# Kernel optimization log

Measured on AMD Instinct MI355X. Metric: run time of the kernel, lower is better.

The kernel has to match this reference:

```python
import jax, jax.numpy as jnp
import numpy as np
from jax import lax

GRID_W, GRID_H = 4, 4
N_NODES = GRID_W * GRID_H  # 16
N_NEIGH = 8
N_CLS = 10
BN_EPS = 1e-5


def _neighbors(i, w, h, mode=8):
    # exact port of Brain.neighbors (ordering matters for the concat)
    size = w * h
    out = []
    if i - w >= 0:
        out.append(i - w)
    if i % w != 0:
        out.append(i - 1)
    if (i + 1) % w != 0:
        out.append(i + 1)
    if i + w < size:
        out.append(i + w)
    if mode == 8:
        if i - w - 1 >= 0 and i % w != 0:
            out.append(i - w - 1)
        if i - w + 1 >= 0 and (i + 1) % w != 0:
            out.append(i - w + 1)
        if i + w - 1 < size and i % w != 0:
            out.append(i + w - 1)
        if i + w + 1 < size and (i + 1) % w != 0:
            out.append(i + w + 1)
    return out


def _neighbor_table():
    idx = np.full((N_NODES, N_NEIGH), 0, dtype=np.int32)
    mask = np.zeros((N_NODES, N_NEIGH), dtype=np.float32)
    for i in range(N_NODES):
        n = _neighbors(i, GRID_W, GRID_H, 8)
        idx[i, :len(n)] = np.array(n, dtype=np.int32)
        mask[i, :len(n)] = 1.0
    return jnp.asarray(idx), jnp.asarray(mask)


def _conv(x, w, b):
    y = lax.conv_general_dilated(x, w, (1, 1), 'SAME',
                                 dimension_numbers=('NCHW', 'OIHW', 'NCHW'))
    return y + b[None, :, None, None]


def _bn_train(x, g, b):
    # BatchNorm2d in training mode (module default): batch statistics
    mean = jnp.mean(x, axis=(0, 2, 3), keepdims=True)
    var = jnp.var(x, axis=(0, 2, 3), keepdims=True)
    xn = (x - mean) * lax.rsqrt(var + BN_EPS)
    return xn * g[None, :, None, None] + b[None, :, None, None]


def _maxpool(x):
    # MaxPool2d(kernel=3, stride=2, padding=1)
    return lax.reduce_window(x, -jnp.inf, lax.max,
                             (1, 1, 3, 3), (1, 1, 2, 2),
                             ((0, 0), (0, 0), (1, 1), (1, 1)))


def setup_inputs() -> dict:
    key = jax.random.key(0)
    ks = jax.random.split(key, 24)
    B = 128
    f32 = jnp.float32

    def rn(k, shape, scale):
        return jax.random.normal(k, shape, dtype=f32) * scale

    inp = {
        'x': rn(ks[0], (B, 3, 64, 64), 1.0),
        'cw1': rn(ks[1], (64, 3, 3, 3), 0.1), 'cb1': jnp.zeros((64,), f32),
        'bn1_g': jnp.ones((64,), f32), 'bn1_b': jnp.zeros((64,), f32),
        'cw2': rn(ks[2], (128, 64, 3, 3), 0.05), 'cb2': jnp.zeros((128,), f32),
        'bn2_g': jnp.ones((128,), f32), 'bn2_b': jnp.zeros((128,), f32),
        'cw3': rn(ks[3], (256, 128, 3, 3), 0.03), 'cb3': jnp.zeros((256,), f32),
        'cw4': rn(ks[4], (256, 256, 3, 3), 0.02), 'cb4': jnp.zeros((256,), f32),
        'cw5': rn(ks[5], (512, 256, 3, 3), 0.02), 'cb5': jnp.zeros((512,), f32),
        'cw6': rn(ks[6], (512, 512, 3, 3), 0.015), 'cb6': jnp.zeros((512,), f32),
        'cw7': rn(ks[7], (512, 512, 3, 3), 0.015), 'cb7': jnp.zeros((512,), f32),
        'W1': rn(ks[8], (N_NODES, 592, 600), 0.04), 'b1': jnp.zeros((N_NODES, 600), f32),
        'W2': rn(ks[9], (N_NODES, 600, N_CLS), 0.04), 'b2': jnp.zeros((N_NODES, N_CLS), f32),
    }
    return inp


def _backbone(x, cw1, cb1, bn1_g, bn1_b, cw2, cb2, bn2_g, bn2_b,
              cw3, cb3, cw4, cb4, cw5, cb5, cw6, cb6, cw7, cb7):
    h = _maxpool(jax.nn.relu(_bn_train(_conv(x, cw1, cb1), bn1_g, bn1_b)))
    h = _maxpool(jax.nn.relu(_bn_train(_conv(h, cw2, cb2), bn2_g, bn2_b)))
    h = jax.nn.relu(_conv(h, cw3, cb3))
    h = _maxpool(jax.nn.relu(_conv(h, cw4, cb4)))
    h = jax.nn.relu(_conv(h, cw5, cb5))
    h = _maxpool(jax.nn.relu(_conv(h, cw6, cb6)))
    h = jax.nn.relu(_conv(h, cw7, cb7))
    return h  # [B, 512, 4, 4]


def _colons(X, W1, b1, W2, b2):
    # X: [16, B, 592] -> softmax probs [16, B, 10]; per-node MLP
    h = jnp.tanh(jnp.einsum('nbi,nio->nbo', X, W1) + b1[:, None, :])
    logits = jnp.einsum('nbh,nho->nbo', h, W2) + b2[:, None, :]
    return jax.nn.softmax(logits, axis=-1)


def reference(x, cw1, cb1, bn1_g, bn1_b, cw2, cb2, bn2_g, bn2_b,
              cw3, cb3, cw4, cb4, cw5, cb5, cw6, cb6, cw7, cb7,
              W1, b1, W2, b2):
    B = x.shape[0]
    conv = _backbone(x, cw1, cb1, bn1_g, bn1_b, cw2, cb2, bn2_g, bn2_b,
                     cw3, cb3, cw4, cb4, cw5, cb5, cw6, cb6, cw7, cb7)
    conv = conv.reshape(B, 512, N_NODES)           # torch.flatten(conv, 2)
    feats = jnp.transpose(conv, (2, 0, 1))         # [16, B, 512]

    # first pass: neighbor slots are all-zero p1..p8
    zeros80 = jnp.zeros((N_NODES, B, N_NEIGH * N_CLS), dtype=x.dtype)
    preds1 = _colons(jnp.concatenate([zeros80, feats], axis=-1), W1, b1, W2, b2)

    # second pass: gather neighbor predictions (zero-padded to 8 slots)
    idx, mask = _neighbor_table()                  # [16,8] int, [16,8] float
    gathered = preds1[idx]                         # [16, 8, B, 10]
    gathered = gathered * mask[:, :, None, None]
    neigh = jnp.transpose(gathered, (0, 2, 1, 3)).reshape(N_NODES, B, N_NEIGH * N_CLS)
    preds2 = _colons(jnp.concatenate([neigh, feats], axis=-1), W1, b1, W2, b2)  # [16, B, 10]

    sum_preds = jnp.mean(preds2, axis=0)           # [B, 10]
    squared_sum_preds = sum_preds * sum_preds
    return squared_sum_preds, preds2
```

## Files before the change

kernel.cpp:

```cpp
#include <hip/hip_runtime.h>
#include <math.h>


#define BN_EPS 1e-5f

typedef _Float16 f16x8 __attribute__((ext_vector_type(8)));
typedef _Float16 f16x4 __attribute__((ext_vector_type(4)));
typedef float    f32x4v __attribute__((ext_vector_type(4)));

constexpr int ilog2c(int x) { return x <= 1 ? 0 : 1 + ilog2c(x >> 1); }

__global__ __launch_bounds__(256)
void wsplit_kernel(const float* __restrict__ w, _Float16* __restrict__ o, int COCI)
{
    const int t = blockIdx.x * 256 + threadIdx.x;
    if (t >= COCI) return;
#pragma unroll
    for (int ph = 0; ph < 9; ++ph)
        o[ph * COCI + t] = (_Float16)w[t * 9 + ph];
}

__global__ void wsplit1_kernel(const float* __restrict__ w, _Float16* __restrict__ o)
{
    const int co = threadIdx.x;
#pragma unroll
    for (int k = 0; k < 32; ++k)
        o[co * 32 + k] = (k < 27) ? (_Float16)w[co * 27 + k] : (_Float16)0.f;
}

__global__ __launch_bounds__(256)
void conv1_mfma_kernel(const float* __restrict__ in, const _Float16* __restrict__ w32,
                       _Float16* __restrict__ out, int B)
{
    __shared__ __align__(16) _Float16 As[64 * 32];
    __shared__ __align__(16) _Float16 Bs[128 * 32];

    const int tid  = threadIdx.x;
    const int pix0 = blockIdx.x * 128;
    const int bn   = tid & 127;
    const int bh   = tid >> 7;
    const int gp   = pix0 + bn;
    const int pb   = gp >> 12;
    const int sp   = gp & 4095;
    const int py   = sp >> 6;
    const int px   = sp & 63;
    const float* inb = in + (size_t)pb * 3 * 4096;

    _Float16 vals[16];
    if (bh == 0) {
#pragma unroll
        for (int u = 0; u < 16; ++u) {
            const int k = u;
            const int ci = k / 9, r = k - ci * 9, ky = r / 3, kx = r - ky * 3;
            const int iy = py + ky - 1, ix = px + kx - 1;
            float v = 0.f;
            if ((unsigned)iy < 64u && (unsigned)ix < 64u)
                v = inb[ci * 4096 + iy * 64 + ix];
            vals[u] = (_Float16)v;
        }
    } else {
#pragma unroll
        for (int u = 0; u < 16; ++u) {
            const int k = 16 + u;
            float v = 0.f;
            if (k < 27) {
                const int ci = k / 9, r = k - ci * 9, ky = r / 3, kx = r - ky * 3;
                const int iy = py + ky - 1, ix = px + kx - 1;
                if ((unsigned)iy < 64u && (unsigned)ix < 64u)
                    v = inb[ci * 4096 + iy * 64 + ix];
            }
            vals[u] = (_Float16)v;
        }
    }
    f16x8 b0, b1;
#pragma unroll
    for (int j = 0; j < 8; ++j) { b0[j] = vals[j]; b1[j] = vals[8 + j]; }
    *(f16x8*)&Bs[bn * 32 + (((2 * bh    ) ^ (bn & 3)) << 3)] = b0;
    *(f16x8*)&Bs[bn * 32 + (((2 * bh + 1) ^ (bn & 3)) << 3)] = b1;

    if (tid < 128) {
        const int arow = tid >> 1, ah = tid & 1;
        const f16x8 a0 = *(const f16x8*)(w32 + arow * 32 + ah * 16);
        const f16x8 a1 = *(const f16x8*)(w32 + arow * 32 + ah * 16 + 8);
        *(f16x8*)&As[arow * 32 + (((2 * ah    ) ^ (arow & 3)) << 3)] = a0;
        *(f16x8*)&As[arow * 32 + (((2 * ah + 1) ^ (arow & 3)) << 3)] = a1;
    }
    __syncthreads();

    const int lane = tid & 63, wv = tid >> 6;
    const int q = lane >> 4, lm = lane & 15;
    const int swz = (q ^ (lm & 3)) << 3;

    f16x8 af[4], bf[2];
#pragma unroll
    for (int ti = 0; ti < 4; ++ti)
        af[ti] = *(const f16x8*)&As[(ti * 16 + lm) * 32 + swz];
#pragma unroll
    for (int tj = 0; tj < 2; ++tj)
        bf[tj] = *(const f16x8*)&Bs[(wv * 32 + tj * 16 + lm) * 32 + swz];

    f32x4v acc[4][2];
#pragma unroll
    for (int ti = 0; ti < 4; ++ti)
#pragma unroll
        for (int tj = 0; tj < 2; ++tj)
            acc[ti][tj] = __builtin_amdgcn_mfma_f32_16x16x32_f16(
                af[ti], bf[tj], (f32x4v)0.f, 0, 0, 0);

#pragma unroll
    for (int tj = 0; tj < 2; ++tj) {
        const int gpix = pix0 + wv * 32 + tj * 16 + lm;
#pragma unroll
        for (int ti = 0; ti < 4; ++ti) {
            const int cob = ti * 16 + q * 4;
            f16x4 h4;
#pragma unroll
            for (int r = 0; r < 4; ++r) h4[r] = (_Float16)acc[ti][tj][r];
            *(f16x4*)&out[(size_t)gpix * 64 + cob] = h4;
        }
    }
}

template <int CI, int CO, int H, int W, int KSPLIT, int EPI>
__global__ __launch_bounds__(256)
void conv_nhwc_kernel(const _Float16* __restrict__ in, const _Float16* __restrict__ w9,
                      const float* __restrict__ bias, _Float16* __restrict__ out,
                      float* __restrict__ part, int B)
{
    constexpr int HW   = H * W;
    constexpr int lgHW = ilog2c(HW);
    constexpr int lgW  = ilog2c(W);

    __shared__ __align__(16) _Float16 As[128 * 32];
    __shared__ __align__(16) _Float16 Bs[128 * 32];

    const int tid  = threadIdx.x;
    const int pix0 = blockIdx.x * 128;
    const int co0  = blockIdx.y * 128;

    const int bn = tid & 127;
    const int bh = tid >> 7;
    const int gp = pix0 + bn;
    const int pb = gp >> lgHW;
    const int sp = gp & (HW - 1);
    const int py = sp >> lgW;
    const int px = sp & (W - 1);

    const int arow = tid >> 1;
    const int ah   = tid & 1;

    const int lane = tid & 63, wv = tid >> 6;
    const int wm = (wv & 1) * 64;
    const int wn = (wv >> 1) * 64;
    const int q = lane >> 4, lm = lane & 15;
    const int swz = (q ^ (lm & 3)) << 3;

    const int bw0 = ((2 * bh    ) ^ (bn & 3)) << 3;
    const int bw1 = ((2 * bh + 1) ^ (bn & 3)) << 3;
    const int aw0 = ((2 * ah    ) ^ (arow & 3)) << 3;
    const int aw1 = ((2 * ah + 1) ^ (arow & 3)) << 3;

    f32x4v acc[4][4];
#pragma unroll
    for (int i = 0; i < 4; ++i)
#pragma unroll
        for (int j = 0; j < 4; ++j) acc[i][j] = (f32x4v)0.f;

    constexpr int CS_TOT = CI / 32;
    constexpr int CS_PER = CS_TOT / KSPLIT;
    const int cs0 = (KSPLIT > 1) ? blockIdx.z * CS_PER : 0;

    for (int ph = 0; ph < 9; ++ph) {
        const int dy = ph / 3 - 1;
        const int dx = ph - (ph / 3) * 3 - 1;
        const int y2 = py + dy;
        const int x2 = px + dx;
        const bool valid = ((unsigned)y2 < (unsigned)H) && ((unsigned)x2 < (unsigned)W);
        const _Float16 msk = valid ? (_Float16)1.f : (_Float16)0.f;
        const int sp2 = valid ? ((y2 << lgW) | x2) : 0;
        const _Float16* bsrc = in + ((size_t)((pb << lgHW) | sp2)) * CI + bh * 16;
        const _Float16* asrc = w9 + ((size_t)(ph * CO) + co0 + arow) * CI + ah * 16;

        for (int cs = cs0; cs < cs0 + CS_PER; ++cs) {
            f16x8 bv0 = *(const f16x8*)(bsrc + cs * 32);
            f16x8 bv1 = *(const f16x8*)(bsrc + cs * 32 + 8);
            const f16x8 av0 = *(const f16x8*)(asrc + cs * 32);
            const f16x8 av1 = *(const f16x8*)(asrc + cs * 32 + 8);

            __syncthreads();
            bv0 *= msk;
            bv1 *= msk;
            *(f16x8*)&Bs[bn * 32 + bw0]   = bv0;
            *(f16x8*)&Bs[bn * 32 + bw1]   = bv1;
            *(f16x8*)&As[arow * 32 + aw0] = av0;
            *(f16x8*)&As[arow * 32 + aw1] = av1;
            __syncthreads();

            f16x8 af[4], bf[4];
#pragma unroll
            for (int ti = 0; ti < 4; ++ti)
                af[ti] = *(const f16x8*)&As[(wm + ti * 16 + lm) * 32 + swz];
#pragma unroll
            for (int tj = 0; tj < 4; ++tj)
                bf[tj] = *(const f16x8*)&Bs[(wn + tj * 16 + lm) * 32 + swz];
#pragma unroll
            for (int ti = 0; ti < 4; ++ti)
#pragma unroll
                for (int tj = 0; tj < 4; ++tj)
                    acc[ti][tj] = __builtin_amdgcn_mfma_f32_16x16x32_f16(
                        af[ti], bf[tj], acc[ti][tj], 0, 0, 0);
        }
    }

    if (EPI == 2) {
        float* pout = part + (size_t)blockIdx.z * ((size_t)B * HW * CO);
#pragma unroll
        for (int tj = 0; tj < 4; ++tj) {
            const int gpix = pix0 + wn + tj * 16 + lm;
#pragma unroll
            for (int ti = 0; ti < 4; ++ti) {
                const int cob = co0 + wm + ti * 16 + q * 4;
                *(float4*)&pout[(size_t)gpix * CO + cob] =
                    make_float4(acc[ti][tj][0], acc[ti][tj][1],
                                acc[ti][tj][2], acc[ti][tj][3]);
            }
        }
    } else {
#pragma unroll
        for (int tj = 0; tj < 4; ++tj) {
            const int gpix = pix0 + wn + tj * 16 + lm;
#pragma unroll
            for (int ti = 0; ti < 4; ++ti) {
                const int cob = co0 + wm + ti * 16 + q * 4;
                f16x4 h4;
                if (EPI == 1) {
                    const float4 bb = *(const float4*)&bias[cob];
                    h4[0] = (_Float16)fmaxf(acc[ti][tj][0] + bb.x, 0.f);
                    h4[1] = (_Float16)fmaxf(acc[ti][tj][1] + bb.y, 0.f);
                    h4[2] = (_Float16)fmaxf(acc[ti][tj][2] + bb.z, 0.f);
                    h4[3] = (_Float16)fmaxf(acc[ti][tj][3] + bb.w, 0.f);
                } else {
#pragma unroll
                    for (int r = 0; r < 4; ++r) h4[r] = (_Float16)acc[ti][tj][r];
                }
                *(f16x4*)&out[(size_t)gpix * CO + cob] = h4;
            }
        }
    }
}

template <int C>
__global__ __launch_bounds__(256)
void bn_stats_nhwc_kernel(const _Float16* __restrict__ in, float* __restrict__ sums,
                          int Ptot)
{
    constexpr int C8 = C / 8;
    constexpr int PS = 256 / C8;
    const int chunk = Ptot / gridDim.x;
    const int c8   = threadIdx.x & (C8 - 1);
    const int poff = threadIdx.x >> ilog2c(C8);
    float s[8], s2[8];
#pragma unroll
    for (int j = 0; j < 8; ++j) { s[j] = 0.f; s2[j] = 0.f; }
    const int p0 = blockIdx.x * chunk;
    for (int p = p0 + poff; p < p0 + chunk; p += PS) {
        const f16x8 v = *(const f16x8*)(in + (size_t)p * C + c8 * 8);
#pragma unroll
        for (int j = 0; j < 8; ++j) {
            const float f = (float)v[j];
            s[j] += f; s2[j] += f * f;
        }
    }
    __shared__ float ls[2 * C];
    for (int i = threadIdx.x; i < 2 * C; i += 256) ls[i] = 0.f;
    __syncthreads();
#pragma unroll
    for (int j = 0; j < 8; ++j) {
        atomicAdd(&ls[c8 * 8 + j], s[j]);
        atomicAdd(&ls[C + c8 * 8 + j], s2[j]);
    }
    __syncthreads();
    for (int i = threadIdx.x; i < 2 * C; i += 256) atomicAdd(&sums[i], ls[i]);
}

template <int C>
__global__ void bn_finalize_kernel(const float* __restrict__ sums,
                                   const float* __restrict__ g,
                                   const float* __restrict__ beta,
                                   float* __restrict__ ss, int Ntot)
{
    const int c = blockIdx.x * 64 + threadIdx.x;
    if (c >= C) return;
    const float inv   = 1.f / (float)Ntot;
    const float mean  = sums[c] * inv;
    const float var   = sums[C + c] * inv - mean * mean;
    const float scale = g[c] * rsqrtf(var + BN_EPS);
    ss[c]     = scale;
    ss[C + c] = beta[c] - mean * scale;
}

template <int C, int Hin, int Win, bool DO_BN>
__global__ __launch_bounds__(256)
void pool_nhwc_kernel(const _Float16* __restrict__ in, const float* __restrict__ ss,
                      _Float16* __restrict__ out, int B)
{
    constexpr int Ho = Hin / 2, Wo = Win / 2, C8 = C / 8;
    constexpr int lgC8 = ilog2c(C8), lgWo = ilog2c(Wo), lgHo = ilog2c(Ho);
    const int t = blockIdx.x * 256 + threadIdx.x;
    const int total = B * Ho * Wo * C8;
    if (t >= total) return;
    const int c8 = t & (C8 - 1);
    const int r1 = t >> lgC8;
    const int ox = r1 & (Wo - 1);
    const int r2 = r1 >> lgWo;
    const int oy = r2 & (Ho - 1);
    const int b  = r2 >> lgHo;

    float sc[8], sh[8];
    if (DO_BN) {
#pragma unroll
        for (int j = 0; j < 8; ++j) {
            sc[j] = ss[c8 * 8 + j];
            sh[j] = ss[C + c8 * 8 + j];
        }
    }
    float m[8];
#pragma unroll
    for (int j = 0; j < 8; ++j) m[j] = -1e30f;

    const int y0 = max(0, 2 * oy - 1), y1 = min(Hin - 1, 2 * oy + 1);
    const int x0 = max(0, 2 * ox - 1), x1 = min(Win - 1, 2 * ox + 1);
    const _Float16* ib = in + ((size_t)b * Hin * Win) * C + c8 * 8;
    for (int iy = y0; iy <= y1; ++iy)
        for (int ix = x0; ix <= x1; ++ix) {
            const f16x8 v = *(const f16x8*)(ib + (size_t)(iy * Win + ix) * C);
#pragma unroll
            for (int j = 0; j < 8; ++j) {
                float f = (float)v[j];
                if (DO_BN) f = f * sc[j] + sh[j];
                m[j] = fmaxf(m[j], f);
            }
        }
    f16x8 o;
#pragma unroll
    for (int j = 0; j < 8; ++j) {
        float f = m[j];
        if (DO_BN) f = fmaxf(f, 0.f);
        o[j] = (_Float16)f;
    }
    *(f16x8*)&out[((size_t)((b << (lgHo + lgWo)) | (oy << lgWo) | ox)) * C + c8 * 8] = o;
}

template <int CO, int Z>
__global__ __launch_bounds__(256)
void sum_bias_relu_nhwc_kernel(const float* __restrict__ part, const float* __restrict__ bias,
                               _Float16* __restrict__ out, int Npix)
{
    const int t = blockIdx.x * 256 + threadIdx.x;
    const int N8 = Npix * CO / 8;
    if (t >= N8) return;
    const size_t i8 = (size_t)t * 8;
    const int c = (int)(i8 & (CO - 1));
    const size_t S = (size_t)Npix * CO;
    float4 x0 = *(const float4*)(part + i8);
    float4 x1 = *(const float4*)(part + i8 + 4);
#pragma unroll
    for (int z = 1; z < Z; ++z) {
        const float4 p0 = *(const float4*)(part + z * S + i8);
        const float4 p1 = *(const float4*)(part + z * S + i8 + 4);
        x0.x += p0.x; x0.y += p0.y; x0.z += p0.z; x0.w += p0.w;
        x1.x += p1.x; x1.y += p1.y; x1.z += p1.z; x1.w += p1.w;
    }
    const float4 b0 = *(const float4*)(bias + c);
    const float4 b1 = *(const float4*)(bias + c + 4);
    f16x8 o;
    o[0] = (_Float16)fmaxf(x0.x + b0.x, 0.f);
    o[1] = (_Float16)fmaxf(x0.y + b0.y, 0.f);
    o[2] = (_Float16)fmaxf(x0.z + b0.z, 0.f);
    o[3] = (_Float16)fmaxf(x0.w + b0.w, 0.f);
    o[4] = (_Float16)fmaxf(x1.x + b1.x, 0.f);
    o[5] = (_Float16)fmaxf(x1.y + b1.y, 0.f);
    o[6] = (_Float16)fmaxf(x1.z + b1.z, 0.f);
    o[7] = (_Float16)fmaxf(x1.w + b1.w, 0.f);
    *(f16x8*)&out[i8] = o;
}

template <int Z>
__global__ __launch_bounds__(256)
void build_x_kernel(const float* __restrict__ part, const float* __restrict__ bias,
                    float* __restrict__ X, int B)
{
    const int t = blockIdx.x * 256 + threadIdx.x;
    if (t >= B * 16 * 128) return;
    const int pix = t >> 7;
    const int c   = (t & 127) * 4;
    const size_t S = (size_t)B * 16 * 512;
    float4 a = *(const float4*)(part + (size_t)pix * 512 + c);
#pragma unroll
    for (int z = 1; z < Z; ++z) {
        const float4 p = *(const float4*)(part + z * S + (size_t)pix * 512 + c);
        a.x += p.x; a.y += p.y; a.z += p.z; a.w += p.w;
    }
    const float4 bb = *(const float4*)(bias + c);
    a.x = fmaxf(a.x + bb.x, 0.f);
    a.y = fmaxf(a.y + bb.y, 0.f);
    a.z = fmaxf(a.z + bb.z, 0.f);
    a.w = fmaxf(a.w + bb.w, 0.f);
    const int b_ = pix >> 4, sp = pix & 15;
    *(float4*)&X[((size_t)(sp * B + b_)) * 592 + 80 + c] = a;
}

template <int K, int XOFF, int WOFF, bool WRITE_PRE, bool ADD_PRE>
__global__ __launch_bounds__(256)
void colon_fc1_kernel(const float* __restrict__ X, const float* __restrict__ W1,
                      const float* __restrict__ b1, float* __restrict__ pre,
                      float* __restrict__ h, int B)
{
    constexpr int N = 600, BK = 16;
    const int n  = blockIdx.z;
    const int m0 = blockIdx.y * 64;
    const int o0 = blockIdx.x * 64;

    __shared__ __align__(16) float As[BK][68];
    __shared__ __align__(16) float Bs[BK][68];

    const int tid = threadIdx.x;
    const int tx = tid & 15, ty = tid >> 4;
    const int a_m = tid >> 2, a_k4 = (tid & 3) * 4;
    const int b_o = tid & 63, b_kr = tid >> 6;

    const float* Xn  = X  + (size_t)n * B * 592;
    const float* W1n = W1 + (size_t)n * 592 * N;

    float acc[4][4];
#pragma unroll
    for (int i = 0; i < 4; ++i)
#pragma unroll
        for (int j = 0; j < 4; ++j) acc[i][j] = 0.f;

    for (int kb = 0; kb < K; kb += BK) {
        const float4 av = *reinterpret_cast<const float4*>(
            &Xn[(size_t)(m0 + a_m) * 592 + XOFF + kb + a_k4]);
        As[a_k4 + 0][a_m] = av.x;
        As[a_k4 + 1][a_m] = av.y;
        As[a_k4 + 2][a_m] = av.z;
        As[a_k4 + 3][a_m] = av.w;
#pragma unroll
        for (int i = 0; i < 4; ++i) {
            const int kl = b_kr + i * 4;
            const int o  = o0 + b_o;
            Bs[kl][b_o] = (o < N) ? W1n[(size_t)(WOFF + kb + kl) * N + o] : 0.f;
        }
        __syncthreads();
#pragma unroll
        for (int kk = 0; kk < BK; ++kk) {
            const float4 a4 = *reinterpret_cast<const float4*>(&As[kk][ty * 4]);
            const float4 b4 = *reinterpret_cast<const float4*>(&Bs[kk][tx * 4]);
            const float a0[4] = {a4.x, a4.y, a4.z, a4.w};
            const float b0[4] = {b4.x, b4.y, b4.z, b4.w};
#pragma unroll
            for (int i = 0; i < 4; ++i)
#pragma unroll
                for (int j = 0; j < 4; ++j)
                    acc[i][j] += a0[i] * b0[j];
        }
        __syncthreads();
    }

#pragma unroll
    for (int i = 0; i < 4; ++i) {
        const int m = m0 + ty * 4 + i;
#pragma unroll
        for (int j = 0; j < 4; ++j) {
            const int o = o0 + tx * 4 + j;
            if (o < N) {
                const size_t oi = ((size_t)(n * B + m)) * N + o;
                float v = acc[i][j] + (ADD_PRE ? pre[oi] : b1[n * N + o]);
                if (WRITE_PRE) pre[oi] = v;
                h[oi] = tanhf(v);
            }
        }
    }
}

__global__ __launch_bounds__(128)
void colon_fc2_kernel(const float* __restrict__ h, const float* __restrict__ W2,
                      const float* __restrict__ b2, float* __restrict__ preds, int B)
{
    const int n = blockIdx.x;
    __shared__ float W2s[6000];
    __shared__ float b2s[10];
    for (int i = threadIdx.x; i < 6000; i += 128) W2s[i] = W2[n * 6000 + i];
    if (threadIdx.x < 10) b2s[threadIdx.x] = b2[n * 10 + threadIdx.x];
    __syncthreads();

    for (int b = threadIdx.x; b < B; b += 128) {
        float l[10];
#pragma unroll
        for (int c = 0; c < 10; ++c) l[c] = b2s[c];
        const float* hp = h + ((size_t)(n * B + b)) * 600;
        for (int k = 0; k < 600; k += 4) {
            const float4 hv = *reinterpret_cast<const float4*>(&hp[k]);
            const float hh[4] = {hv.x, hv.y, hv.z, hv.w};
#pragma unroll
            for (int u = 0; u < 4; ++u)
#pragma unroll
                for (int c = 0; c < 10; ++c)
                    l[c] += hh[u] * W2s[(k + u) * 10 + c];
        }
        float mx = l[0];
#pragma unroll
        for (int c = 1; c < 10; ++c) mx = fmaxf(mx, l[c]);
        float s = 0.f;
#pragma unroll
        for (int c = 0; c < 10; ++c) { l[c] = expf(l[c] - mx); s += l[c]; }
        const float inv = 1.f / s;
        float* pp = preds + ((size_t)(n * B + b)) * 10;
#pragma unroll
        for (int c = 0; c < 10; ++c) pp[c] = l[c] * inv;
    }
}

__global__ __launch_bounds__(256)
void fill_neigh_kernel(const float* __restrict__ preds1, float* __restrict__ X, int B)
{
    const int t = blockIdx.x * 256 + threadIdx.x;
    if (t >= 16 * B * 80) return;
    const int c = t % 10;
    const int j = (t / 10) & 7;
    const int b = (t / 80) % B;
    const int n = t / (80 * B);

    int lst[8];
    int cnt = 0;
    const int w = 4, sz = 16, i = n;
    if (i - w >= 0)                                lst[cnt++] = i - w;
    if (i % w != 0)                                lst[cnt++] = i - 1;
    if ((i + 1) % w != 0)                          lst[cnt++] = i + 1;
    if (i + w < sz)                                lst[cnt++] = i + w;
    if (i - w - 1 >= 0 && i % w != 0)              lst[cnt++] = i - w - 1;
    if (i - w + 1 >= 0 && (i + 1) % w != 0)        lst[cnt++] = i - w + 1;
    if (i + w - 1 < sz && i % w != 0)              lst[cnt++] = i + w - 1;
    if (i + w + 1 < sz && (i + 1) % w != 0)        lst[cnt++] = i + w + 1;

    float v = 0.f;
    if (j < cnt) v = preds1[((size_t)(lst[j] * B + b)) * 10 + c];
    X[((size_t)(n * B + b)) * 592 + j * 10 + c] = v;
}

__global__ __launch_bounds__(256)
void final_out_kernel(const float* __restrict__ preds2, float* __restrict__ out0, int B)
{
    const int t = blockIdx.x * 256 + threadIdx.x;
    if (t >= B * 10) return;
    const int b = t / 10, c = t % 10;
    float s = 0.f;
#pragma unroll
    for (int n = 0; n < 16; ++n)
        s += preds2[((size_t)(n * B + b)) * 10 + c];
    const float m = s * (1.f / 16.f);
    out0[t] = m * m;
}

extern "C" void kernel_launch(void* const* d_in, const int* in_sizes, int n_in,
                              void* d_out, int out_size, void* d_ws, size_t ws_size,
                              hipStream_t stream)
{
    const float* x    = (const float*)d_in[0];
    const float* cw1  = (const float*)d_in[1];
    const float* bn1g = (const float*)d_in[3];
    const float* bn1b = (const float*)d_in[4];
    const float* cw2  = (const float*)d_in[5];
    const float* bn2g = (const float*)d_in[7];
    const float* bn2b = (const float*)d_in[8];
    const float* cw3  = (const float*)d_in[9];
    const float* cb3  = (const float*)d_in[10];
    const float* cw4  = (const float*)d_in[11];
    const float* cb4  = (const float*)d_in[12];
    const float* cw5  = (const float*)d_in[13];
    const float* cb5  = (const float*)d_in[14];
    const float* cw6  = (const float*)d_in[15];
    const float* cb6  = (const float*)d_in[16];
    const float* cw7  = (const float*)d_in[17];
    const float* cb7  = (const float*)d_in[18];
    const float* W1   = (const float*)d_in[19];
    const float* b1   = (const float*)d_in[20];
    const float* W2   = (const float*)d_in[21];
    const float* b2   = (const float*)d_in[22];

    const int B = in_sizes[0] / (3 * 64 * 64);

    float* ws = (float*)d_ws;
    float*     P    = ws;
    _Float16*  A    = (_Float16*)(ws + 16777216);
    _Float16*  Bb   = (_Float16*)(ws + 33554432);
    _Float16*  wreg = (_Float16*)(ws + 41943040);
    float*     Xb   = ws + 45371392;
    float*     hb   = ws + 46583808;
    float*     preb = ws + 47812608;
    float*     small= ws + 49041408;
    float* sums1  = small;
    float* sums2  = small + 256;
    float* ss1    = small + 1024;
    float* ss2    = small + 1536;
    float* preds1 = small + 2048;

    _Float16* w1f  = wreg;
    _Float16* w9c2 = wreg + 2048;
    _Float16* w9c3 = w9c2 + 73728;
    _Float16* w9c4 = w9c3 + 294912;
    _Float16* w9c5 = w9c4 + 589824;
    _Float16* w9c6 = w9c5 + 1179648;
    _Float16* w9c7 = w9c6 + 2359296;

    float* out0   = (float*)d_out;
    float* preds2 = (float*)d_out + (size_t)B * 10;

    hipMemsetAsync(small, 0, 512 * sizeof(float), stream);

    wsplit1_kernel<<<1, 64, 0, stream>>>(cw1, w1f);
    wsplit_kernel<<<(128 * 64  + 255) / 256, 256, 0, stream>>>(cw2, w9c2, 128 * 64);
    wsplit_kernel<<<(256 * 128 + 255) / 256, 256, 0, stream>>>(cw3, w9c3, 256 * 128);
    wsplit_kernel<<<(256 * 256 + 255) / 256, 256, 0, stream>>>(cw4, w9c4, 256 * 256);
    wsplit_kernel<<<(512 * 256 + 255) / 256, 256, 0, stream>>>(cw5, w9c5, 512 * 256);
    wsplit_kernel<<<(512 * 512 + 255) / 256, 256, 0, stream>>>(cw6, w9c6, 512 * 512);
    wsplit_kernel<<<(512 * 512 + 255) / 256, 256, 0, stream>>>(cw7, w9c7, 512 * 512);

    conv1_mfma_kernel<<<B * 4096 / 128, 256, 0, stream>>>(x, w1f, A, B);
    bn_stats_nhwc_kernel<64><<<512, 256, 0, stream>>>(A, sums1, B * 4096);
    bn_finalize_kernel<64><<<1, 64, 0, stream>>>(sums1, bn1g, bn1b, ss1, B * 4096);
    pool_nhwc_kernel<64, 64, 64, true>
        <<<(B * 1024 * 8 + 255) / 256, 256, 0, stream>>>(A, ss1, Bb, B);

    conv_nhwc_kernel<64, 128, 32, 32, 1, 0>
        <<<dim3(B * 1024 / 128, 1), 256, 0, stream>>>(Bb, w9c2, nullptr, A, nullptr, B);
    bn_stats_nhwc_kernel<128><<<256, 256, 0, stream>>>(A, sums2, B * 1024);
    bn_finalize_kernel<128><<<2, 64, 0, stream>>>(sums2, bn2g, bn2b, ss2, B * 1024);
    pool_nhwc_kernel<128, 32, 32, true>
        <<<(B * 256 * 16 + 255) / 256, 256, 0, stream>>>(A, ss2, Bb, B);

    conv_nhwc_kernel<128, 256, 16, 16, 1, 1>
        <<<dim3(B * 256 / 128, 2), 256, 0, stream>>>(Bb, w9c3, cb3, A, nullptr, B);
    conv_nhwc_kernel<256, 256, 16, 16, 1, 1>
        <<<dim3(B * 256 / 128, 2), 256, 0, stream>>>(A, w9c4, cb4, Bb, nullptr, B);
    pool_nhwc_kernel<256, 16, 16, false>
        <<<(B * 64 * 32 + 255) / 256, 256, 0, stream>>>(Bb, nullptr, A, B);

    conv_nhwc_kernel<256, 512, 8, 8, 2, 2>
        <<<dim3(B * 64 / 128, 4, 2), 256, 0, stream>>>(A, w9c5, nullptr, nullptr, P, B);
    sum_bias_relu_nhwc_kernel<512, 2>
        <<<(B * 64 * 512 / 8 + 255) / 256, 256, 0, stream>>>(P, cb5, Bb, B * 64);

    conv_nhwc_kernel<512, 512, 8, 8, 2, 2>
        <<<dim3(B * 64 / 128, 4, 2), 256, 0, stream>>>(Bb, w9c6, nullptr, nullptr, P, B);
    sum_bias_relu_nhwc_kernel<512, 2>
        <<<(B * 64 * 512 / 8 + 255) / 256, 256, 0, stream>>>(P, cb6, A, B * 64);
    pool_nhwc_kernel<512, 8, 8, false>
        <<<(B * 16 * 64 + 255) / 256, 256, 0, stream>>>(A, nullptr, Bb, B);

    conv_nhwc_kernel<512, 512, 4, 4, 8, 2>
        <<<dim3(B * 16 / 128, 4, 8), 256, 0, stream>>>(Bb, w9c7, nullptr, nullptr, P, B);

    build_x_kernel<8><<<(B * 16 * 128 + 255) / 256, 256, 0, stream>>>(P, cb7, Xb, B);

    colon_fc1_kernel<512, 80, 80, true, false>
        <<<dim3(10, B / 64, 16), 256, 0, stream>>>(Xb, W1, b1, preb, hb, B);
    colon_fc2_kernel<<<16, 128, 0, stream>>>(hb, W2, b2, preds1, B);

    fill_neigh_kernel<<<(16 * B * 80 + 255) / 256, 256, 0, stream>>>(preds1, Xb, B);
    colon_fc1_kernel<80, 0, 0, false, true>
        <<<dim3(10, B / 64, 16), 256, 0, stream>>>(Xb, W1, b1, preb, hb, B);
    colon_fc2_kernel<<<16, 128, 0, stream>>>(hb, W2, b2, preds2, B);

    final_out_kernel<<<(B * 10 + 255) / 256, 256, 0, stream>>>(preds2, out0, B);
}
```

Before: 734.8 us.

## Use MFMA for colon FC1 and drop LDS staging of conv activations

Replaces the fp32 SIMT FC1 GEMMs with fp16 MFMA kernels. W1 is transposed and padded to 640 outputs per node on device, and activations are written as fp16. The conv kernel is reworked so activation fragments load straight from global memory into registers with masking, and only the weight tile goes through double-buffered LDS, which halves the barriers per step. This lowers LDS traffic and sync cost but adds uncoalesced direct global loads. It also adds per-call W1 transpose work and fp16 rounding in FC1.

```diff
diff --git a/kernel.cpp b/kernel.cpp
--- a/kernel.cpp
+++ b/kernel.cpp
@@ -26,6 +26,48 @@
 #pragma unroll
     for (int k = 0; k < 32; ++k)
         o[co * 32 + k] = (k < 27) ? (_Float16)w[co * 27 + k] : (_Float16)0.f;
+}
+
+__global__ __launch_bounds__(256)
+void w1t_kernel(const float* __restrict__ W1, _Float16* __restrict__ Tf,
+                _Float16* __restrict__ Tn)
+{
+    __shared__ float T[64][65];
+    const int n  = blockIdx.z;
+    const int o0 = blockIdx.y * 64;
+    const int k0 = blockIdx.x * 64;
+    const int tid = threadIdx.x;
+    const int c  = tid & 63;
+    const int r4 = tid >> 6;
+    const float* Wn = W1 + (size_t)n * 592 * 600;
+#pragma unroll
+    for (int rep = 0; rep < 16; ++rep) {
+        const int kr = rep * 4 + r4;
+        const int k = k0 + kr, o = o0 + c;
+        float v = 0.f;
+        if (k < 592 && o < 600) v = Wn[k * 600 + o];
+        T[kr][c] = v;
+    }
+    __syncthreads();
+#pragma unroll
+    for (int rep = 0; rep < 16; ++rep) {
+        const int orr = rep * 4 + r4;
+        const int o = o0 + orr;
+        const int k = k0 + c;
+        const float v = T[c][orr];
+        if (k >= 80 && k < 592)
+            Tf[((size_t)(n * 640 + o)) * 512 + (k - 80)] = (_Float16)v;
+        if (k < 96)
+            Tn[((size_t)(n * 640 + o)) * 96 + k] = (k < 80) ? (_Float16)v : (_Float16)0.f;
+    }
+}
+
+__global__ void b1pad_kernel(const float* __restrict__ b1, float* __restrict__ b1p)
+{
+    const int t = blockIdx.x * 256 + threadIdx.x;
+    if (t >= 16 * 640) return;
+    const int n = t / 640, o = t - n * 640;
+    b1p[t] = (o < 600) ? b1[n * 600 + o] : 0.f;
 }
 
 __global__ __launch_bounds__(256)
@@ -123,42 +165,39 @@
 
 template <int CI, int CO, int H, int W, int KSPLIT, int EPI>
 __global__ __launch_bounds__(256)
-void conv_nhwc_kernel(const _Float16* __restrict__ in, const _Float16* __restrict__ w9,
-                      const float* __restrict__ bias, _Float16* __restrict__ out,
-                      float* __restrict__ part, int B)
+void conv_bd_kernel(const _Float16* __restrict__ in, const _Float16* __restrict__ w9,
+                    const float* __restrict__ bias, _Float16* __restrict__ out,
+                    float* __restrict__ part, int B)
 {
     constexpr int HW   = H * W;
     constexpr int lgHW = ilog2c(HW);
     constexpr int lgW  = ilog2c(W);
 
-    __shared__ __align__(16) _Float16 As[128 * 32];
-    __shared__ __align__(16) _Float16 Bs[128 * 32];
+    __shared__ __align__(16) _Float16 As[2][128 * 32];
 
     const int tid  = threadIdx.x;
     const int pix0 = blockIdx.x * 128;
     const int co0  = blockIdx.y * 128;
 
-    const int bn = tid & 127;
-    const int bh = tid >> 7;
-    const int gp = pix0 + bn;
-    const int pb = gp >> lgHW;
-    const int sp = gp & (HW - 1);
-    const int py = sp >> lgW;
-    const int px = sp & (W - 1);
-
-    const int arow = tid >> 1;
-    const int ah   = tid & 1;
-
     const int lane = tid & 63, wv = tid >> 6;
-    const int wm = (wv & 1) * 64;
-    const int wn = (wv >> 1) * 64;
+    const int wm = (wv & 1) * 64, wn = (wv >> 1) * 64;
     const int q = lane >> 4, lm = lane & 15;
     const int swz = (q ^ (lm & 3)) << 3;
 
-    const int bw0 = ((2 * bh    ) ^ (bn & 3)) << 3;
-    const int bw1 = ((2 * bh + 1) ^ (bn & 3)) << 3;
+    const int arow = tid >> 1, ah = tid & 1;
     const int aw0 = ((2 * ah    ) ^ (arow & 3)) << 3;
     const int aw1 = ((2 * ah + 1) ^ (arow & 3)) << 3;
+    const _Float16* abase = w9 + ((size_t)(co0 + arow)) * CI + ah * 16;
+
+    int pbq[4], pyq[4], pxq[4];
+#pragma unroll
+    for (int tj = 0; tj < 4; ++tj) {
+        const int gp = pix0 + wn + tj * 16 + lm;
+        pbq[tj] = gp >> lgHW;
+        const int sp = gp & (HW - 1);
+        pyq[tj] = sp >> lgW;
+        pxq[tj] = sp & (W - 1);
+    }
 
     f32x4v acc[4][4];
 #pragma unroll
@@ -170,45 +209,59 @@
     constexpr int CS_PER = CS_TOT / KSPLIT;
     const int cs0 = (KSPLIT > 1) ? blockIdx.z * CS_PER : 0;
 
+    int buf = 0;
     for (int ph = 0; ph < 9; ++ph) {
         const int dy = ph / 3 - 1;
         const int dx = ph - (ph / 3) * 3 - 1;
-        const int y2 = py + dy;
-        const int x2 = px + dx;
-        const bool valid = ((unsigned)y2 < (unsigned)H) && ((unsigned)x2 < (unsigned)W);
-        const _Float16 msk = valid ? (_Float16)1.f : (_Float16)0.f;
-        const int sp2 = valid ? ((y2 << lgW) | x2) : 0;
-        const _Float16* bsrc = in + ((size_t)((pb << lgHW) | sp2)) * CI + bh * 16;
-        const _Float16* asrc = w9 + ((size_t)(ph * CO) + co0 + arow) * CI + ah * 16;
-
-        for (int cs = cs0; cs < cs0 + CS_PER; ++cs) {
-            f16x8 bv0 = *(const f16x8*)(bsrc + cs * 32);
-            f16x8 bv1 = *(const f16x8*)(bsrc + cs * 32 + 8);
-            const f16x8 av0 = *(const f16x8*)(asrc + cs * 32);
-            const f16x8 av1 = *(const f16x8*)(asrc + cs * 32 + 8);
-
+        const _Float16* bb[4];
+        f16x8 mskv[4];
+#pragma unroll
+        for (int tj = 0; tj < 4; ++tj) {
+            const int y2 = pyq[tj] + dy, x2 = pxq[tj] + dx;
+            const bool valid = ((unsigned)y2 < (unsigned)H) && ((unsigned)x2 < (unsigned)W);
+            const int sp2 = valid ? ((y2 << lgW) | x2) : 0;
+            bb[tj] = in + ((size_t)((pbq[tj] << lgHW) | sp2)) * CI + q * 8 + cs0 * 32;
+            const _Float16 m = valid ? (_Float16)1.f : (_Float16)0.f;
+#pragma unroll
+            for (int j = 0; j < 8; ++j) mskv[tj][j] = m;
+        }
+        const _Float16* aph = abase + (size_t)ph * CO * CI + cs0 * 32;
+
+        {
+            const f16x8 a0 = *(const f16x8*)(aph);
+            const f16x8 a1 = *(const f16x8*)(aph + 8);
             __syncthreads();
-            bv0 *= msk;
-            bv1 *= msk;
-            *(f16x8*)&Bs[bn * 32 + bw0]   = bv0;
-            *(f16x8*)&Bs[bn * 32 + bw1]   = bv1;
-            *(f16x8*)&As[arow * 32 + aw0] = av0;
-            *(f16x8*)&As[arow * 32 + aw1] = av1;
+            *(f16x8*)&As[buf][arow * 32 + aw0] = a0;
+            *(f16x8*)&As[buf][arow * 32 + aw1] = a1;
+        }
+        for (int cs = 0; cs < CS_PER; ++cs) {
+            f16x8 bfr[4];
+#pragma unroll
+            for (int tj = 0; tj < 4; ++tj)
+                bfr[tj] = *(const f16x8*)(bb[tj] + cs * 32);
+            f16x8 aN0, aN1;
+            if (cs + 1 < CS_PER) {
+                aN0 = *(const f16x8*)(aph + (cs + 1) * 32);
+                aN1 = *(const f16x8*)(aph + (cs + 1) * 32 + 8);
+            }
             __syncthreads();
-
-            f16x8 af[4], bf[4];
+            f16x8 afr[4];
 #pragma unroll
             for (int ti = 0; ti < 4; ++ti)
-                af[ti] = *(const f16x8*)&As[(wm + ti * 16 + lm) * 32 + swz];
-#pragma unroll
-            for (int tj = 0; tj < 4; ++tj)
-                bf[tj] = *(const f16x8*)&Bs[(wn + tj * 16 + lm) * 32 + swz];
+                afr[ti] = *(const f16x8*)&As[buf][(wm + ti * 16 + lm) * 32 + swz];
+#pragma unroll
+            for (int tj = 0; tj < 4; ++tj) bfr[tj] *= mskv[tj];
 #pragma unroll
             for (int ti = 0; ti < 4; ++ti)
 #pragma unroll
                 for (int tj = 0; tj < 4; ++tj)
                     acc[ti][tj] = __builtin_amdgcn_mfma_f32_16x16x32_f16(
-                        af[ti], bf[tj], acc[ti][tj], 0, 0, 0);
+                        afr[ti], bfr[tj], acc[ti][tj], 0, 0, 0);
+            if (cs + 1 < CS_PER) {
+                *(f16x8*)&As[buf ^ 1][arow * 32 + aw0] = aN0;
+                *(f16x8*)&As[buf ^ 1][arow * 32 + aw1] = aN1;
+                buf ^= 1;
+            }
         }
     }
 
@@ -234,11 +287,11 @@
                 const int cob = co0 + wm + ti * 16 + q * 4;
                 f16x4 h4;
                 if (EPI == 1) {
-                    const float4 bb = *(const float4*)&bias[cob];
-                    h4[0] = (_Float16)fmaxf(acc[ti][tj][0] + bb.x, 0.f);
-                    h4[1] = (_Float16)fmaxf(acc[ti][tj][1] + bb.y, 0.f);
-                    h4[2] = (_Float16)fmaxf(acc[ti][tj][2] + bb.z, 0.f);
-                    h4[3] = (_Float16)fmaxf(acc[ti][tj][3] + bb.w, 0.f);
+                    const float4 bb4 = *(const float4*)&bias[cob];
+                    h4[0] = (_Float16)fmaxf(acc[ti][tj][0] + bb4.x, 0.f);
+                    h4[1] = (_Float16)fmaxf(acc[ti][tj][1] + bb4.y, 0.f);
+                    h4[2] = (_Float16)fmaxf(acc[ti][tj][2] + bb4.z, 0.f);
+                    h4[3] = (_Float16)fmaxf(acc[ti][tj][3] + bb4.w, 0.f);
                 } else {
 #pragma unroll
                     for (int r = 0; r < 4; ++r) h4[r] = (_Float16)acc[ti][tj][r];
@@ -387,8 +440,8 @@
 
 template <int Z>
 __global__ __launch_bounds__(256)
-void build_x_kernel(const float* __restrict__ part, const float* __restrict__ bias,
-                    float* __restrict__ X, int B)
+void build_xf_kernel(const float* __restrict__ part, const float* __restrict__ bias,
+                     _Float16* __restrict__ Xf, int B)
 {
     const int t = blockIdx.x * 256 + threadIdx.x;
     if (t >= B * 16 * 128) return;
@@ -402,83 +455,103 @@
         a.x += p.x; a.y += p.y; a.z += p.z; a.w += p.w;
     }
     const float4 bb = *(const float4*)(bias + c);
-    a.x = fmaxf(a.x + bb.x, 0.f);
-    a.y = fmaxf(a.y + bb.y, 0.f);
-    a.z = fmaxf(a.z + bb.z, 0.f);
-    a.w = fmaxf(a.w + bb.w, 0.f);
+    f16x4 o4;
+    o4[0] = (_Float16)fmaxf(a.x + bb.x, 0.f);
+    o4[1] = (_Float16)fmaxf(a.y + bb.y, 0.f);
+    o4[2] = (_Float16)fmaxf(a.z + bb.z, 0.f);
+    o4[3] = (_Float16)fmaxf(a.w + bb.w, 0.f);
     const int b_ = pix >> 4, sp = pix & 15;
-    *(float4*)&X[((size_t)(sp * B + b_)) * 592 + 80 + c] = a;
-}
-
-template <int K, int XOFF, int WOFF, bool WRITE_PRE, bool ADD_PRE>
-__global__ __launch_bounds__(256)
-void colon_fc1_kernel(const float* __restrict__ X, const float* __restrict__ W1,
-                      const float* __restrict__ b1, float* __restrict__ pre,
-                      float* __restrict__ h, int B)
-{
-    constexpr int N = 600, BK = 16;
-    const int n  = blockIdx.z;
-    const int m0 = blockIdx.y * 64;
-    const int o0 = blockIdx.x * 64;
-
-    __shared__ __align__(16) float As[BK][68];
-    __shared__ __align__(16) float Bs[BK][68];
+    *(f16x4*)&Xf[((size_t)(sp * B + b_)) * 512 + c] = o4;
+}
+
+template <int K, bool PASS2>
+__global__ __launch_bounds__(256)
+void fc1_mfma_kernel(const _Float16* __restrict__ Xf, const _Float16* __restrict__ W1T,
+                     const float* __restrict__ b1p, float* __restrict__ pre,
+                     float* __restrict__ h, int B)
+{
+    __shared__ __align__(16) _Float16 As[2][128 * 32];
+    __shared__ __align__(16) _Float16 Bs[2][128 * 32];
 
     const int tid = threadIdx.x;
-    const int tx = tid & 15, ty = tid >> 4;
-    const int a_m = tid >> 2, a_k4 = (tid & 3) * 4;
-    const int b_o = tid & 63, b_kr = tid >> 6;
-
-    const float* Xn  = X  + (size_t)n * B * 592;
-    const float* W1n = W1 + (size_t)n * 592 * N;
-
-    float acc[4][4];
+    const int o0  = blockIdx.x * 128;
+    const int n   = blockIdx.y;
+
+    const int lane = tid & 63, wv = tid >> 6;
+    const int wm = (wv & 1) * 64, wn = (wv >> 1) * 64;
+    const int q = lane >> 4, lm = lane & 15;
+    const int swz = (q ^ (lm & 3)) << 3;
+
+    const int arow = tid >> 1, ah = tid & 1;
+    const int aw0 = ((2 * ah    ) ^ (arow & 3)) << 3;
+    const int aw1 = ((2 * ah + 1) ^ (arow & 3)) << 3;
+
+    const _Float16* asrc = W1T + ((size_t)(n * 640 + o0 + arow)) * K + ah * 16;
+    const _Float16* bsrc = Xf  + ((size_t)(n * 128 + arow)) * K + ah * 16;
+
+    f32x4v acc[4][4];
 #pragma unroll
     for (int i = 0; i < 4; ++i)
 #pragma unroll
-        for (int j = 0; j < 4; ++j) acc[i][j] = 0.f;
-
-    for (int kb = 0; kb < K; kb += BK) {
-        const float4 av = *reinterpret_cast<const float4*>(
-            &Xn[(size_t)(m0 + a_m) * 592 + XOFF + kb + a_k4]);
-        As[a_k4 + 0][a_m] = av.x;
-        As[a_k4 + 1][a_m] = av.y;
-        As[a_k4 + 2][a_m] = av.z;
-        As[a_k4 + 3][a_m] = av.w;
-#pragma unroll
-        for (int i = 0; i < 4; ++i) {
-            const int kl = b_kr + i * 4;
-            const int o  = o0 + b_o;
-            Bs[kl][b_o] = (o < N) ? W1n[(size_t)(WOFF + kb + kl) * N + o] : 0.f;
+        for (int j = 0; j < 4; ++j) acc[i][j] = (f32x4v)0.f;
+
+    constexpr int S = K / 32;
+    {
+        const f16x8 a0 = *(const f16x8*)(asrc);
+        const f16x8 a1 = *(const f16x8*)(asrc + 8);
+        const f16x8 b0 = *(const f16x8*)(bsrc);
+        const f16x8 b1 = *(const f16x8*)(bsrc + 8);
+        *(f16x8*)&As[0][arow * 32 + aw0] = a0;
+        *(f16x8*)&As[0][arow * 32 + aw1] = a1;
+        *(f16x8*)&Bs[0][arow * 32 + aw0] = b0;
+        *(f16x8*)&Bs[0][arow * 32 + aw1] = b1;
+    }
+    int buf = 0;
+    for (int s = 0; s < S; ++s) {
+        f16x8 aN0, aN1, bN0, bN1;
+        if (s + 1 < S) {
+            aN0 = *(const f16x8*)(asrc + (s + 1) * 32);
+            aN1 = *(const f16x8*)(asrc + (s + 1) * 32 + 8);
+            bN0 = *(const f16x8*)(bsrc + (s + 1) * 32);
+            bN1 = *(const f16x8*)(bsrc + (s + 1) * 32 + 8);
         }
         __syncthreads();
-#pragma unroll
-        for (int kk = 0; kk < BK; ++kk) {
-            const float4 a4 = *reinterpret_cast<const float4*>(&As[kk][ty * 4]);
-            const float4 b4 = *reinterpret_cast<const float4*>(&Bs[kk][tx * 4]);
-            const float a0[4] = {a4.x, a4.y, a4.z, a4.w};
-            const float b0[4] = {b4.x, b4.y, b4.z, b4.w};
-#pragma unroll
-            for (int i = 0; i < 4; ++i)
-#pragma unroll
-                for (int j = 0; j < 4; ++j)
-                    acc[i][j] += a0[i] * b0[j];
-        }
-        __syncthreads();
-    }
-
-#pragma unroll
-    for (int i = 0; i < 4; ++i) {
-        const int m = m0 + ty * 4 + i;
-#pragma unroll
-        for (int j = 0; j < 4; ++j) {
-            const int o = o0 + tx * 4 + j;
-            if (o < N) {
-                const size_t oi = ((size_t)(n * B + m)) * N + o;
-                float v = acc[i][j] + (ADD_PRE ? pre[oi] : b1[n * N + o]);
-                if (WRITE_PRE) pre[oi] = v;
-                h[oi] = tanhf(v);
-            }
+        f16x8 afr[4], bfr[4];
+#pragma unroll
+        for (int ti = 0; ti < 4; ++ti)
+            afr[ti] = *(const f16x8*)&As[buf][(wm + ti * 16 + lm) * 32 + swz];
+#pragma unroll
+        for (int tj = 0; tj < 4; ++tj)
+            bfr[tj] = *(const f16x8*)&Bs[buf][(wn + tj * 16 + lm) * 32 + swz];
+#pragma unroll
+        for (int ti = 0; ti < 4; ++ti)
+#pragma unroll
+            for (int tj = 0; tj < 4; ++tj)
+                acc[ti][tj] = __builtin_amdgcn_mfma_f32_16x16x32_f16(
+                    afr[ti], bfr[tj], acc[ti][tj], 0, 0, 0);
+        if (s + 1 < S) {
+            *(f16x8*)&As[buf ^ 1][arow * 32 + aw0] = aN0;
+            *(f16x8*)&As[buf ^ 1][arow * 32 + aw1] = aN1;
+            *(f16x8*)&Bs[buf ^ 1][arow * 32 + aw0] = bN0;
+            *(f16x8*)&Bs[buf ^ 1][arow * 32 + aw1] = bN1;
+            buf ^= 1;
+        }
+    }
+
+#pragma unroll
+    for (int tj = 0; tj < 4; ++tj) {
+        const int m = wn + tj * 16 + lm;
+#pragma unroll
+        for (int ti = 0; ti < 4; ++ti) {
+            const int o = o0 + wm + ti * 16 + q * 4;
+            const size_t oi = ((size_t)(n * 128 + m)) * 640 + o;
+            float4 base;
+            if (PASS2) base = *(const float4*)&pre[oi];
+            else       base = *(const float4*)&b1p[n * 640 + o];
+            float4 v = make_float4(acc[ti][tj][0] + base.x, acc[ti][tj][1] + base.y,
+                                   acc[ti][tj][2] + base.z, acc[ti][tj][3] + base.w);
+            if (!PASS2) *(float4*)&pre[oi] = v;
+            *(float4*)&h[oi] = make_float4(tanhf(v.x), tanhf(v.y), tanhf(v.z), tanhf(v.w));
         }
     }
 }
@@ -498,7 +571,7 @@
         float l[10];
 #pragma unroll
         for (int c = 0; c < 10; ++c) l[c] = b2s[c];
-        const float* hp = h + ((size_t)(n * B + b)) * 600;
+        const float* hp = h + ((size_t)(n * B + b)) * 640;
         for (int k = 0; k < 600; k += 4) {
             const float4 hv = *reinterpret_cast<const float4*>(&hp[k]);
             const float hh[4] = {hv.x, hv.y, hv.z, hv.w};
@@ -522,30 +595,31 @@
 }
 
 __global__ __launch_bounds__(256)
-void fill_neigh_kernel(const float* __restrict__ preds1, float* __restrict__ X, int B)
+void fill_neigh_kernel(const float* __restrict__ preds1, _Float16* __restrict__ Xn, int B)
 {
     const int t = blockIdx.x * 256 + threadIdx.x;
-    if (t >= 16 * B * 80) return;
-    const int c = t % 10;
-    const int j = (t / 10) & 7;
-    const int b = (t / 80) % B;
-    const int n = t / (80 * B);
-
-    int lst[8];
-    int cnt = 0;
-    const int w = 4, sz = 16, i = n;
-    if (i - w >= 0)                                lst[cnt++] = i - w;
-    if (i % w != 0)                                lst[cnt++] = i - 1;
-    if ((i + 1) % w != 0)                          lst[cnt++] = i + 1;
-    if (i + w < sz)                                lst[cnt++] = i + w;
-    if (i - w - 1 >= 0 && i % w != 0)              lst[cnt++] = i - w - 1;
-    if (i - w + 1 >= 0 && (i + 1) % w != 0)        lst[cnt++] = i - w + 1;
-    if (i + w - 1 < sz && i % w != 0)              lst[cnt++] = i + w - 1;
-    if (i + w + 1 < sz && (i + 1) % w != 0)        lst[cnt++] = i + w + 1;
+    if (t >= 16 * B * 96) return;
+    const int col = t % 96;
+    const int b   = (t / 96) % B;
+    const int n   = t / (96 * B);
 
     float v = 0.f;
-    if (j < cnt) v = preds1[((size_t)(lst[j] * B + b)) * 10 + c];
-    X[((size_t)(n * B + b)) * 592 + j * 10 + c] = v;
+    if (col < 80) {
+        const int j = col / 10, c = col - j * 10;
+        int lst[8];
+        int cnt = 0;
+        const int w = 4, sz = 16, i = n;
+        if (i - w >= 0)                                lst[cnt++] = i - w;
+        if (i % w != 0)                                lst[cnt++] = i - 1;
+        if ((i + 1) % w != 0)                          lst[cnt++] = i + 1;
+        if (i + w < sz)                                lst[cnt++] = i + w;
+        if (i - w - 1 >= 0 && i % w != 0)              lst[cnt++] = i - w - 1;
+        if (i - w + 1 >= 0 && (i + 1) % w != 0)        lst[cnt++] = i - w + 1;
+        if (i + w - 1 < sz && i % w != 0)              lst[cnt++] = i + w - 1;
+        if (i + w + 1 < sz && (i + 1) % w != 0)        lst[cnt++] = i + w + 1;
+        if (j < cnt) v = preds1[((size_t)(lst[j] * B + b)) * 10 + c];
+    }
+    Xn[t] = (_Float16)v;
 }
 
 __global__ __launch_bounds__(256)
@@ -592,13 +666,17 @@
 
     float* ws = (float*)d_ws;
     float*     P    = ws;
-    _Float16*  A    = (_Float16*)(ws + 16777216);
-    _Float16*  Bb   = (_Float16*)(ws + 33554432);
-    _Float16*  wreg = (_Float16*)(ws + 41943040);
-    float*     Xb   = ws + 45371392;
-    float*     hb   = ws + 46583808;
-    float*     preb = ws + 47812608;
-    float*     small= ws + 49041408;
+    _Float16*  A    = (_Float16*)(ws + 8388608);
+    _Float16*  Bb   = (_Float16*)(ws + 25165824);
+    _Float16*  wreg = (_Float16*)(ws + 33554432);
+    _Float16*  W1Tf = (_Float16*)(ws + 36984832);
+    _Float16*  W1Tn = (_Float16*)(ws + 39606272);
+    _Float16*  Xf16 = (_Float16*)(ws + 40097792);
+    _Float16*  Xn16 = (_Float16*)(ws + 40622080);
+    float*     b1p  = ws + 40720384;
+    float*     preb = ws + 40730624;
+    float*     hb   = ws + 42041344;
+    float*     small= ws + 43352064;
     float* sums1  = small;
     float* sums2  = small + 256;
     float* ss1    = small + 1024;
@@ -625,6 +703,8 @@
     wsplit_kernel<<<(512 * 256 + 255) / 256, 256, 0, stream>>>(cw5, w9c5, 512 * 256);
     wsplit_kernel<<<(512 * 512 + 255) / 256, 256, 0, stream>>>(cw6, w9c6, 512 * 512);
     wsplit_kernel<<<(512 * 512 + 255) / 256, 256, 0, stream>>>(cw7, w9c7, 512 * 512);
+    w1t_kernel<<<dim3(10, 10, 16), 256, 0, stream>>>(W1, W1Tf, W1Tn);
+    b1pad_kernel<<<(16 * 640 + 255) / 256, 256, 0, stream>>>(b1, b1p);
 
     conv1_mfma_kernel<<<B * 4096 / 128, 256, 0, stream>>>(x, w1f, A, B);
     bn_stats_nhwc_kernel<64><<<512, 256, 0, stream>>>(A, sums1, B * 4096);
@@ -632,44 +712,44 @@
     pool_nhwc_kernel<64, 64, 64, true>
         <<<(B * 1024 * 8 + 255) / 256, 256, 0, stream>>>(A, ss1, Bb, B);
 
-    conv_nhwc_kernel<64, 128, 32, 32, 1, 0>
+    conv_bd_kernel<64, 128, 32, 32, 1, 0>
         <<<dim3(B * 1024 / 128, 1), 256, 0, stream>>>(Bb, w9c2, nullptr, A, nullptr, B);
     bn_stats_nhwc_kernel<128><<<256, 256, 0, stream>>>(A, sums2, B * 1024);
     bn_finalize_kernel<128><<<2, 64, 0, stream>>>(sums2, bn2g, bn2b, ss2, B * 1024);
     pool_nhwc_kernel<128, 32, 32, true>
         <<<(B * 256 * 16 + 255) / 256, 256, 0, stream>>>(A, ss2, Bb, B);
 
-    conv_nhwc_kernel<128, 256, 16, 16, 1, 1>
+    conv_bd_kernel<128, 256, 16, 16, 1, 1>
         <<<dim3(B * 256 / 128, 2), 256, 0, stream>>>(Bb, w9c3, cb3, A, nullptr, B);
-    conv_nhwc_kernel<256, 256, 16, 16, 1, 1>
+    conv_bd_kernel<256, 256, 16, 16, 1, 1>
         <<<dim3(B * 256 / 128, 2), 256, 0, stream>>>(A, w9c4, cb4, Bb, nullptr, B);
     pool_nhwc_kernel<256, 16, 16, false>
         <<<(B * 64 * 32 + 255) / 256, 256, 0, stream>>>(Bb, nullptr, A, B);
 
-    conv_nhwc_kernel<256, 512, 8, 8, 2, 2>
+    conv_bd_kernel<256, 512, 8, 8, 2, 2>
         <<<dim3(B * 64 / 128, 4, 2), 256, 0, stream>>>(A, w9c5, nullptr, nullptr, P, B);
     sum_bias_relu_nhwc_kernel<512, 2>
         <<<(B * 64 * 512 / 8 + 255) / 256, 256, 0, stream>>>(P, cb5, Bb, B * 64);
 
-    conv_nhwc_kernel<512, 512, 8, 8, 2, 2>
+    conv_bd_kernel<512, 512, 8, 8, 2, 2>
         <<<dim3(B * 64 / 128, 4, 2), 256, 0, stream>>>(Bb, w9c6, nullptr, nullptr, P, B);
     sum_bias_relu_nhwc_kernel<512, 2>
         <<<(B * 64 * 512 / 8 + 255) / 256, 256, 0, stream>>>(P, cb6, A, B * 64);
     pool_nhwc_kernel<512, 8, 8, false>
         <<<(B * 16 * 64 + 255) / 256, 256, 0, stream>>>(A, nullptr, Bb, B);
 
-    conv_nhwc_kernel<512, 512, 4, 4, 8, 2>
+    conv_bd_kernel<512, 512, 4, 4, 8, 2>
         <<<dim3(B * 16 / 128, 4, 8), 256, 0, stream>>>(Bb, w9c7, nullptr, nullptr, P, B);
 
-    build_x_kernel<8><<<(B * 16 * 128 + 255) / 256, 256, 0, stream>>>(P, cb7, Xb, B);
-
-    colon_fc1_kernel<512, 80, 80, true, false>
-        <<<dim3(10, B / 64, 16), 256, 0, stream>>>(Xb, W1, b1, preb, hb, B);
+    build_xf_kernel<8><<<(B * 16 * 128 + 255) / 256, 256, 0, stream>>>(P, cb7, Xf16, B);
+
+    fc1_mfma_kernel<512, false>
+        <<<dim3(5, 16), 256, 0, stream>>>(Xf16, W1Tf, b1p, preb, hb, B);
     colon_fc2_kernel<<<16, 128, 0, stream>>>(hb, W2, b2, preds1, B);
 
-    fill_neigh_kernel<<<(16 * B * 80 + 255) / 256, 256, 0, stream>>>(preds1, Xb, B);
-    colon_fc1_kernel<80, 0, 0, false, true>
-        <<<dim3(10, B / 64, 16), 256, 0, stream>>>(Xb, W1, b1, preb, hb, B);
+    fill_neigh_kernel<<<(16 * B * 96 + 255) / 256, 256, 0, stream>>>(preds1, Xn16, B);
+    fc1_mfma_kernel<96, true>
+        <<<dim3(5, 16), 256, 0, stream>>>(Xn16, W1Tn, b1p, preb, hb, B);
     colon_fc2_kernel<<<16, 128, 0, stream>>>(hb, W2, b2, preds2, B);
 
     final_out_kernel<<<(B * 10 + 255) / 256, 256, 0, stream>>>(preds2, out0, B);
```

Result: no change. 740.3 us (+0.8%).
